# Kernel tuning notes

Hardware: AMD Instinct MI355X
Metric: run time of the kernel (lower is better)

## Reference

```python
import jax, jax.numpy as jnp
import numpy as np

N = 207      # nodes (hardcoded in source)
D = 128      # hid_dim
H = 8        # attention heads
C = D // H   # head dim
L = 4        # num_layers
B = 16       # batch
NO = 3       # number of orbits
SZ = 69      # orbit size
EPS = 1e-5
SLOPE = 0.2  # GATv2 leaky_relu negative slope


def _cat_matrix():
    # edge category for pair (i,j): off-diag -> pos_i*NO+pos_j, diag -> NO^2+pos_i
    pos = np.arange(N) // SZ
    c = pos[:, None] * NO + pos[None, :]
    np.fill_diagonal(c, NO * NO + pos)
    return c  # [N, N] int


def setup_inputs() -> dict:
    key = jax.random.key(0)
    ks = jax.random.split(key, 16)
    s = 0.05
    rn = lambda k, shape: jax.random.normal(k, shape, jnp.float32) * s
    return {
        "x": jax.random.normal(ks[0], (B, N, 6), jnp.float32),
        "cat": jnp.asarray(_cat_matrix(), jnp.int32),          # [N,N] edge categories
        "emb": rn(ks[1], (NO * NO + NO, D)),                   # edge embedding table
        "in1_W": rn(ks[2], (D, 6)), "in1_b": jnp.zeros((D,)),
        "ln1_g": jnp.ones((D,)), "ln1_b": jnp.zeros((D,)),
        "in2_W": rn(ks[3], (D, D)), "in2_b": jnp.zeros((D,)),
        "ln2_g": jnp.ones((D,)), "ln2_b": jnp.zeros((D,)),
        "Wl": rn(ks[4], (L, D, D)), "bl": jnp.zeros((L, D)),   # GATv2 lin_l (source)
        "Wr": rn(ks[5], (L, D, D)), "br": jnp.zeros((L, D)),   # GATv2 lin_r (target)
        "We": rn(ks[6], (L, D, D)),                            # GATv2 lin_edge (no bias)
        "att": rn(ks[7], (L, H, C)),                           # attention vector
        "cb": jnp.zeros((L, D)),                               # conv output bias
        "pW": rn(ks[8], (L, D, D)), "pb": jnp.zeros((L, D)),   # projection layers
        "lng": jnp.ones((L, D)), "lnb": jnp.zeros((L, D)),     # per-layer LayerNorm
        "oW": rn(ks[9], (2, D)), "ob": jnp.zeros((2,)),        # output layer
    }


def _ln(x, g, b):
    m = x.mean(-1, keepdims=True)
    v = ((x - m) ** 2).mean(-1, keepdims=True)
    return (x - m) * jax.lax.rsqrt(v + EPS) * g + b


def _fwd(cat, x, emb, in1_W, in1_b, ln1_g, ln1_b, in2_W, in2_b, ln2_g, ln2_b,
         Wl, bl, Wr, br, We, att, cb, pW, pb, lng, lnb, oW, ob):
    # input MLP: Linear -> LN -> ReLU -> Linear -> LN
    h = jax.nn.relu(_ln(x @ in1_W.T + in1_b, ln1_g, ln1_b))
    h = _ln(h @ in2_W.T + in2_b, ln2_g, ln2_b)                 # [B,N,D]
    e_all = emb[cat]                                           # [N,N,D] per-edge embedding
    for l in range(L):
        h_prev = h
        gs = (h @ Wl[l].T + bl[l]).reshape(B, N, H, C)         # source transform
        gd = (h @ Wr[l].T + br[l]).reshape(B, N, H, C)         # target transform
        ee = (e_all @ We[l].T).reshape(N, N, H, C)             # edge transform
        # per-edge GATv2 score: edge (i -> j), i source, j target
        z = jax.nn.leaky_relu(gs[:, :, None] + gd[:, None, :] + ee[None], SLOPE)  # [B,i,j,H,C]
        a = jnp.einsum('bijhc,hc->bijh', z, att[l])
        a = jax.nn.softmax(a, axis=1)                          # softmax over sources per target
        o = jnp.einsum('bijh,bihc->bjhc', a, gs).reshape(B, N, D) + cb[l]
        h = h_prev + jax.nn.relu(_ln(o @ pW[l].T + pb[l], lng[l], lnb[l]))
    return h @ oW.T + ob                                       # [B,N,2]


def reference(x, cat, emb, in1_W, in1_b, ln1_g, ln1_b, in2_W, in2_b, ln2_g, ln2_b,
              Wl, bl, Wr, br, We, att, cb, pW, pb, lng, lnb, oW, ob):
    return _fwd(cat, x, emb, in1_W, in1_b, ln1_g, ln1_b, in2_W, in2_b, ln2_g, ln2_b,
                Wl, bl, Wr, br, We, att, cb, pW, pb, lng, lnb, oW, ob)
```

## Files before the change

### kernel.cpp

```cpp
#include <hip/hip_runtime.h>
#include <hip/hip_bf16.h>

#define NN 207
#define DD 128
#define LL 4
#define BB 16
#define ROWS (BB*NN)
#define RB 8
#define LBLK (ROWS/RB)
#define EPSV 1e-5f
#define SLOPE 0.2f
#define GT4B (32*208*4)

#define BFBITS 0x3F803F80u

template<bool BF>
__device__ __forceinline__ float ldin(const void* p, int i) {
    if (BF) {
        unsigned short u = ((const unsigned short*)p)[i];
        return __uint_as_float(((unsigned)u) << 16);
    } else {
        return ((const float*)p)[i];
    }
}

template<bool BF>
__device__ __forceinline__ float4 ld4(const void* p, int q4) {
    if (BF) {
        uint2 u = ((const uint2*)p)[q4];
        float4 r;
        r.x = __uint_as_float(u.x << 16);
        r.y = __uint_as_float(u.x & 0xFFFF0000u);
        r.z = __uint_as_float(u.y << 16);
        r.w = __uint_as_float(u.y & 0xFFFF0000u);
        return r;
    } else {
        return ((const float4*)p)[q4];
    }
}

template<bool BF>
__device__ __forceinline__ void ldw32(const void* W, int base, float* w) {
    if (BF) {
        const uint4* p = (const uint4*)((const unsigned short*)W + base);
#pragma unroll
        for (int q = 0; q < 4; q++) {
            uint4 u = p[q];
            w[q*8+0] = __uint_as_float(u.x << 16);
            w[q*8+1] = __uint_as_float(u.x & 0xFFFF0000u);
            w[q*8+2] = __uint_as_float(u.y << 16);
            w[q*8+3] = __uint_as_float(u.y & 0xFFFF0000u);
            w[q*8+4] = __uint_as_float(u.z << 16);
            w[q*8+5] = __uint_as_float(u.z & 0xFFFF0000u);
            w[q*8+6] = __uint_as_float(u.w << 16);
            w[q*8+7] = __uint_as_float(u.w & 0xFFFF0000u);
        }
    } else {
        const float4* p = (const float4*)((const float*)W + base);
#pragma unroll
        for (int q = 0; q < 8; q++) {
            float4 u = p[q];
            w[q*4+0] = u.x; w[q*4+1] = u.y; w[q*4+2] = u.z; w[q*4+3] = u.w;
        }
    }
}

template<bool BF>
__device__ __forceinline__ float rowdot(const void* W, int rowbase, const float* sh) {
    float acc = 0.f;
    if (BF) {
        const uint4* p = (const uint4*)((const unsigned short*)W + rowbase);
#pragma unroll
        for (int q = 0; q < DD / 8; q++) {
            uint4 u = p[q];
            const float* s = sh + q * 8;
            acc += __uint_as_float(u.x << 16)        * s[0];
            acc += __uint_as_float(u.x & 0xFFFF0000u) * s[1];
            acc += __uint_as_float(u.y << 16)        * s[2];
            acc += __uint_as_float(u.y & 0xFFFF0000u) * s[3];
            acc += __uint_as_float(u.z << 16)        * s[4];
            acc += __uint_as_float(u.z & 0xFFFF0000u) * s[5];
            acc += __uint_as_float(u.w << 16)        * s[6];
            acc += __uint_as_float(u.w & 0xFFFF0000u) * s[7];
        }
    } else {
        const float4* p = (const float4*)((const float*)W + rowbase);
#pragma unroll
        for (int q = 0; q < DD / 4; q++) {
            float4 u = p[q];
            const float* s = sh + q * 4;
            acc += u.x * s[0]; acc += u.y * s[1]; acc += u.z * s[2]; acc += u.w * s[3];
        }
    }
    return acc;
}

template<bool BF>
__device__ void et_body(float* sh, const void* emb, const void* We, float* et) {
    int l = blockIdx.x / 12, c = blockIdx.x % 12, d = threadIdx.x;
    sh[d] = ldin<BF>(emb, c * DD + d);
    __syncthreads();
    et[(l * 12 + c) * DD + d] = rowdot<BF>(We, l * DD * DD + d * DD, sh);
}
__global__ void k_et(const unsigned* bits, const void* emb, const void* We, float* et) {
    __shared__ __align__(16) float smem[DD];
    if (bits[0] == BFBITS) et_body<true>(smem, emb, We, et);
    else                   et_body<false>(smem, emb, We, et);
}

#define LING_SMEM (RB*DD + RB*132 + 16 + RB*128)
template<bool BF>
__device__ void linG_body(float* smem, int hasPre, int epi, int hasNext,
                          const float* __restrict__ in,
                          const void* xin, const void* W1, const void* b1,
                          const void* g1, const void* bv1,
                          const void* W, int wOff,
                          const void* bias, const void* g, const void* bv, int dOff,
                          const void* Wl, const void* bl, const void* Wr, const void* br,
                          int nwOff, int nbOff,
                          float* __restrict__ h, float* __restrict__ gs,
                          float* __restrict__ gd, float* __restrict__ gs_t4,
                          const void* oW, const void* ob, void* out) {
    float* sh    = smem;
    float* so    = sh + RB * DD;
    float* stats = so + RB * 132;
    float* s_gs  = stats + 16;
    float* s_x   = s_gs;
    int r0 = blockIdx.x * RB;
    int t = threadIdx.x, d = t & 127, half = t >> 7;
    int rr2 = t >> 5, l32 = t & 31;

    if (hasPre) {
        if (t < RB * 6) s_x[t] = ldin<BF>(xin, r0 * 6 + t);
        __syncthreads();
        if (half == 0) {
            float w6[6];
#pragma unroll
            for (int k = 0; k < 6; k++) w6[k] = ldin<BF>(W1, d * 6 + k);
            float b0p = ldin<BF>(b1, d);
#pragma unroll
            for (int rr = 0; rr < RB; rr++) {
                float a = b0p;
#pragma unroll
                for (int k = 0; k < 6; k++) a += w6[k] * s_x[rr * 6 + k];
                so[rr * 132 + d] = a;
            }
        }
        __syncthreads();
        float s = 0.f, sq = 0.f;
#pragma unroll
        for (int k = 0; k < 4; k++) { float v = so[rr2 * 132 + l32 + 32 * k]; s += v; sq += v * v; }
        s += __shfl_xor(s, 1); s += __shfl_xor(s, 2); s += __shfl_xor(s, 4);
        s += __shfl_xor(s, 8); s += __shfl_xor(s, 16);
        sq += __shfl_xor(sq, 1); sq += __shfl_xor(sq, 2); sq += __shfl_xor(sq, 4);
        sq += __shfl_xor(sq, 8); sq += __shfl_xor(sq, 16);
        if (l32 == 0) {
            float mean = s * (1.f / DD);
            float var = sq * (1.f / DD) - mean * mean;
            stats[rr2 * 2] = mean; stats[rr2 * 2 + 1] = rsqrtf(var + EPSV);
        }
        __syncthreads();
        float gvp = ldin<BF>(g1, d), bbp = ldin<BF>(bv1, d);
#pragma unroll
        for (int rr = 0; rr < 4; rr++) {
            int row = half * 4 + rr;
            float v = (so[row * 132 + d] - stats[row * 2]) * stats[row * 2 + 1] * gvp + bbp;
            sh[row * DD + d] = fmaxf(v, 0.f);
        }
        __syncthreads();
    } else {
        ((float4*)sh)[t] = ((const float4*)(in + (size_t)r0 * DD))[t];
        __syncthreads();
    }

    float acc[4];
    float b0 = ldin<BF>(bias, dOff + d);
#pragma unroll
    for (int rr = 0; rr < 4; rr++) acc[rr] = b0;
#pragma unroll
    for (int c = 0; c < 4; c++) {
        float w[32];
        ldw32<BF>(W, wOff + d * DD + c * 32, w);
#pragma unroll
        for (int rr = 0; rr < 4; rr++) {
            const float* s = sh + (half * 4 + rr) * DD + c * 32;
            float a = acc[rr];
#pragma unroll
            for (int k = 0; k < 32; k++) a += s[k] * w[k];
            acc[rr] = a;
        }
    }
    __syncthreads();
#pragma unroll
    for (int rr = 0; rr < 4; rr++) so[(half * 4 + rr) * 132 + d] = acc[rr];
    __syncthreads();
    {
        float s = 0.f, sq = 0.f;
#pragma unroll
        for (int k = 0; k < 4; k++) { float v = so[rr2 * 132 + l32 + 32 * k]; s += v; sq += v * v; }
        s += __shfl_xor(s, 1); s += __shfl_xor(s, 2); s += __shfl_xor(s, 4);
        s += __shfl_xor(s, 8); s += __shfl_xor(s, 16);
        sq += __shfl_xor(sq, 1); sq += __shfl_xor(sq, 2); sq += __shfl_xor(sq, 4);
        sq += __shfl_xor(sq, 8); sq += __shfl_xor(sq, 16);
        if (l32 == 0) {
            float mean = s * (1.f / DD);
            float var = sq * (1.f / DD) - mean * mean;
            stats[rr2 * 2] = mean; stats[rr2 * 2 + 1] = rsqrtf(var + EPSV);
        }
    }
    __syncthreads();
    float gv = ldin<BF>(g, dOff + d), bb = ldin<BF>(bv, dOff + d);
#pragma unroll
    for (int rr = 0; rr < 4; rr++) {
        int row = half * 4 + rr;
        int rg = r0 + row;
        float v = (so[row * 132 + d] - stats[row * 2]) * stats[row * 2 + 1] * gv + bb;
        float hn;
        if (epi) hn = h[(size_t)rg * DD + d] + fmaxf(v, 0.f);
        else     hn = v;
        h[(size_t)rg * DD + d] = hn;
        sh[row * DD + d] = hn;
    }
    __syncthreads();
    if (!hasNext) {
        float s0 = 0.f, s1 = 0.f;
#pragma unroll
        for (int k = 0; k < 4; k++) {
            int dd = l32 + 32 * k;
            float hv = sh[rr2 * DD + dd];
            s0 += hv * ldin<BF>(oW, dd);
            s1 += hv * ldin<BF>(oW, DD + dd);
        }
        s0 += __shfl_xor(s0, 1); s0 += __shfl_xor(s0, 2); s0 += __shfl_xor(s0, 4);
        s0 += __shfl_xor(s0, 8); s0 += __shfl_xor(s0, 16);
        s1 += __shfl_xor(s1, 1); s1 += __shfl_xor(s1, 2); s1 += __shfl_xor(s1, 4);
        s1 += __shfl_xor(s1, 8); s1 += __shfl_xor(s1, 16);
        if (l32 == 0) {
            int rg = r0 + rr2;
            float v0 = s0 + ldin<BF>(ob, 0);
            float v1 = s1 + ldin<BF>(ob, 1);
            if (BF) {
                ((__hip_bfloat16*)out)[rg * 2 + 0] = __float2bfloat16(v0);
                ((__hip_bfloat16*)out)[rg * 2 + 1] = __float2bfloat16(v1);
            } else {
                ((float*)out)[rg * 2 + 0] = v0;
                ((float*)out)[rg * 2 + 1] = v1;
            }
        }
        return;
    }
    {
        const void* Wm = half ? Wr : Wl;
        const void* bm = half ? br : bl;
        float acc2[RB];
        float bn = ldin<BF>(bm, nbOff + d);
#pragma unroll
        for (int rr = 0; rr < RB; rr++) acc2[rr] = bn;
#pragma unroll
        for (int c = 0; c < 4; c++) {
            float w[32];
            ldw32<BF>(Wm, nwOff + d * DD + c * 32, w);
#pragma unroll
            for (int rr = 0; rr < RB; rr++) {
                const float* s = sh + rr * DD + c * 32;
                float a = acc2[rr];
#pragma unroll
                for (int k = 0; k < 32; k++) a += s[k] * w[k];
                acc2[rr] = a;
            }
        }
        if (half) {
#pragma unroll
            for (int rr = 0; rr < RB; rr++) gd[(size_t)(r0 + rr) * DD + d] = acc2[rr];
        } else {
#pragma unroll
            for (int rr = 0; rr < RB; rr++) {
                gs[(size_t)(r0 + rr) * DD + d] = acc2[rr];
                s_gs[rr * DD + d] = acc2[rr];
            }
        }
    }
    __syncthreads();
    {
        int d4 = t >> 3, iL = t & 7;
        int rg = r0 + iL;
        int bb2 = rg / NN, ii = rg - bb2 * NN;
        float4 v;
        v.x = s_gs[iL * DD + d4 * 4 + 0];
        v.y = s_gs[iL * DD + d4 * 4 + 1];
        v.z = s_gs[iL * DD + d4 * 4 + 2];
        v.w = s_gs[iL * DD + d4 * 4 + 3];
        ((float4*)(gs_t4 + (size_t)bb2 * GT4B))[d4 * 208 + ii] = v;
    }
}
__global__ void k_linG(const unsigned* bits, int hasPre, int epi, int hasNext,
                       const float* in,
                       const void* xin, const void* W1, const void* b1,
                       const void* g1, const void* bv1,
                       const void* W, int wOff,
                       const void* bias, const void* g, const void* bv, int dOff,
                       const void* Wl, const void* bl, const void* Wr, const void* br,
                       int nwOff, int nbOff,
                       float* h, float* gs, float* gd, float* gs_t4,
                       const void* oW, const void* ob, void* out) {
    __shared__ __align__(16) float smem[LING_SMEM];
    if (bits[0] == BFBITS)
        linG_body<true>(smem, hasPre, epi, hasNext, in, xin, W1, b1, g1, bv1,
                        W, wOff, bias, g, bv, dOff,
                        Wl, bl, Wr, br, nwOff, nbOff, h, gs, gd, gs_t4, oW, ob, out);
    else
        linG_body<false>(smem, hasPre, epi, hasNext, in, xin, W1, b1, g1, bv1,
                         W, wOff, bias, g, bv, dOff,
                         Wl, bl, Wr, br, nwOff, nbOff, h, gs, gd, gs_t4, oW, ob, out);
}

#define ATTN_SMEM (12*132 + 8*212 + 8 + 128 + 207)
template<bool BF>
__device__ void attn_body(float* smem, int l, const float* __restrict__ gs,
                          const float* __restrict__ gd, const float* __restrict__ et,
                          const float* __restrict__ gs_t4, const int* __restrict__ cat,
                          const void* att, const void* cb, float* __restrict__ o) {
    float* s_ge   = smem;
    float* s_pe   = s_ge + 12 * 132;
    float* s_inv  = s_pe + 8 * 212;
    float* s_part = s_inv + 8;
    int*   s_cat  = (int*)(s_part + 128);
    int p = blockIdx.x;
    int r = (p & 7) * (ROWS / 8) + (p >> 3);
    int t = threadIdx.x, d = t & 127, seg = t >> 7;
    int b = r / NN, j = r - b * NN;
    for (int idx = t; idx < NN; idx += 256) s_cat[idx] = cat[idx * NN + j];
    for (int idx = t; idx < 12 * DD; idx += 256) {
        int c = idx >> 7, k = idx & 127;
        s_ge[c * 132 + k] = et[l * 12 * DD + idx] + gd[(size_t)r * DD + k];
    }
    __syncthreads();
    const float* gsb = gs + (size_t)b * NN * DD;
    if (t < NN) {
        const float4* gt = ((const float4*)(gs_t4 + (size_t)b * GT4B)) + t;
        const float4* ge = (const float4*)(s_ge + s_cat[t] * 132);
        float acc[8];
#pragma unroll
        for (int hh = 0; hh < 8; hh++) acc[hh] = 0.f;
#pragma unroll
        for (int q = 0; q < 32; q++) {
            float4 g4 = gt[q * 208];
            float4 e4 = ge[q];
            float4 a4 = ld4<BF>(att, l * 32 + q);
            float z0 = g4.x + e4.x, z1 = g4.y + e4.y, z2 = g4.z + e4.z, z3 = g4.w + e4.w;
            z0 = fmaxf(z0, SLOPE * z0); z1 = fmaxf(z1, SLOPE * z1);
            z2 = fmaxf(z2, SLOPE * z2); z3 = fmaxf(z3, SLOPE * z3);
            acc[q >> 2] += a4.x * z0 + a4.y * z1 + a4.z * z2 + a4.w * z3;
        }
#pragma unroll
        for (int hh = 0; hh < 8; hh++) s_pe[hh * 212 + t] = acc[hh];
    }
    __syncthreads();
    if (t < 128) {
        int hh = t >> 4, l16 = t & 15;
        float vals[13]; float mx = -1e30f;
#pragma unroll
        for (int k = 0; k < 13; k++) {
            int i = l16 + 16 * k;
            vals[k] = (i < NN) ? s_pe[hh * 212 + i] : -1e30f;
            mx = fmaxf(mx, vals[k]);
        }
        mx = fmaxf(mx, __shfl_xor(mx, 1)); mx = fmaxf(mx, __shfl_xor(mx, 2));
        mx = fmaxf(mx, __shfl_xor(mx, 4)); mx = fmaxf(mx, __shfl_xor(mx, 8));
        float sum = 0.f;
#pragma unroll
        for (int k = 0; k < 13; k++) {
            int i = l16 + 16 * k;
            float e = (i < NN) ? __expf(vals[k] - mx) : 0.f;
            if (i < 208) s_pe[hh * 212 + i] = e;
            sum += e;
        }
        sum += __shfl_xor(sum, 1); sum += __shfl_xor(sum, 2);
        sum += __shfl_xor(sum, 4); sum += __shfl_xor(sum, 8);
        if (l16 == 0) s_inv[hh] = 1.f / sum;
    }
    __syncthreads();
    {
        int hh = d >> 4;
        const float* ep = s_pe + hh * 212;
        const float* gp = gsb + d;
        float a0 = 0.f, a1 = 0.f, a2 = 0.f, a3 = 0.f;
        int i = seg * 104;
        int iend = seg ? NN : 104;
        for (; i + 8 <= iend; i += 8) {
            float g0 = gp[(i+0)*DD], g1 = gp[(i+1)*DD], g2 = gp[(i+2)*DD], g3 = gp[(i+3)*DD];
            float g4 = gp[(i+4)*DD], g5 = gp[(i+5)*DD], g6 = gp[(i+6)*DD], g7 = gp[(i+7)*DD];
            a0 = fmaf(ep[i+0], g0, a0); a1 = fmaf(ep[i+1], g1, a1);
            a2 = fmaf(ep[i+2], g2, a2); a3 = fmaf(ep[i+3], g3, a3);
            a0 = fmaf(ep[i+4], g4, a0); a1 = fmaf(ep[i+5], g5, a1);
            a2 = fmaf(ep[i+6], g6, a2); a3 = fmaf(ep[i+7], g7, a3);
        }
        for (; i < iend; i++) a0 = fmaf(ep[i], gp[i * DD], a0);
        float part = a0 + a1 + a2 + a3;
        if (seg) s_part[d] = part;
        __syncthreads();
        if (!seg) o[(size_t)r * DD + d] = (part + s_part[d]) * s_inv[hh] + ldin<BF>(cb, l * DD + d);
    }
}
__global__ void __launch_bounds__(256, 4)
k_attn(const unsigned* bits, int l, const float* gs, const float* gd, const float* et,
       const float* gs_t4, const int* cat, const void* att, const void* cb,
       float* o) {
    __shared__ __align__(16) float smem[ATTN_SMEM];
    if (bits[0] == BFBITS) attn_body<true>(smem, l, gs, gd, et, gs_t4, cat, att, cb, o);
    else                   attn_body<false>(smem, l, gs, gd, et, gs_t4, cat, att, cb, o);
}

extern "C" void kernel_launch(void* const* d_in, const int* in_sizes, int n_in,
                              void* d_out, int out_size, void* d_ws, size_t ws_size,
                              hipStream_t stream) {
    const void* x     = d_in[0];
    const int*  cat   = (const int*)d_in[1];
    const void* emb   = d_in[2];
    const void* in1W  = d_in[3];
    const void* in1b  = d_in[4];
    const void* ln1g  = d_in[5];
    const void* ln1b  = d_in[6];
    const void* in2W  = d_in[7];
    const void* in2b  = d_in[8];
    const void* ln2g  = d_in[9];
    const void* ln2b  = d_in[10];
    const void* Wl    = d_in[11];
    const void* bl    = d_in[12];
    const void* Wr    = d_in[13];
    const void* br    = d_in[14];
    const void* We    = d_in[15];
    const void* att   = d_in[16];
    const void* cb    = d_in[17];
    const void* pW    = d_in[18];
    const void* pb    = d_in[19];
    const void* lng   = d_in[20];
    const void* lnb   = d_in[21];
    const void* oW    = d_in[22];
    const void* ob    = d_in[23];

    const unsigned* bits = (const unsigned*)ln1g;

    float* ws  = (float*)d_ws;
    float* h     = ws + 16;
    float* gs    = h    + ROWS * DD;
    float* gd    = gs   + ROWS * DD;
    float* o     = gd   + ROWS * DD;
    float* et    = o    + ROWS * DD;
    float* gs_t4 = et   + LL * 12 * DD;

    k_et<<<LL * 12, DD, 0, stream>>>(bits, emb, We, et);
    k_linG<<<LBLK, 256, 0, stream>>>(bits, 1, 0, 1, (const float*)nullptr,
                                     x, in1W, in1b, ln1g, ln1b,
                                     in2W, 0, in2b, ln2g, ln2b, 0,
                                     Wl, bl, Wr, br, 0, 0,
                                     h, gs, gd, gs_t4, oW, ob, d_out);
    for (int l = 0; l < LL; l++) {
        k_attn<<<ROWS, 256, 0, stream>>>(bits, l, gs, gd, et, gs_t4, cat, att, cb, o);
        k_linG<<<LBLK, 256, 0, stream>>>(bits, 0, 1, (l < LL - 1) ? 1 : 0, o,
                                         x, in1W, in1b, ln1g, ln1b,
                                         pW, l * DD * DD, pb, lng, lnb, l * DD,
                                         Wl, bl, Wr, br, (l + 1) * DD * DD, (l + 1) * DD,
                                         h, gs, gd, gs_t4, oW, ob, d_out);
    }
}
```

Measured before the change: 334.7 us.

## Pre-transpose linear weights to fp32 k-major layout for coalesced loads

Adds a prologue kernel that transposes the in2, projection, lin_l and lin_r weights into a float workspace laid out [k][d]. The linG matmuls then read one weight per k that is coalesced across threads, with activations read as float4 from shared memory. Previously each thread loaded its own 128-wide weight row, so accesses were strided across the wavefront. This costs one extra launch and extra workspace memory per call, and in the bf16 case it doubles the bytes read per weight.

```diff
diff --git a/kernel.cpp b/kernel.cpp
--- a/kernel.cpp
+++ b/kernel.cpp
@@ -11,6 +11,7 @@
 #define EPSV 1e-5f
 #define SLOPE 0.2f
 #define GT4B (32*208*4)
+#define WTM  16384
 
 #define BFBITS 0x3F803F80u
 
@@ -40,32 +41,6 @@
 }
 
 template<bool BF>
-__device__ __forceinline__ void ldw32(const void* W, int base, float* w) {
-    if (BF) {
-        const uint4* p = (const uint4*)((const unsigned short*)W + base);
-#pragma unroll
-        for (int q = 0; q < 4; q++) {
-            uint4 u = p[q];
-            w[q*8+0] = __uint_as_float(u.x << 16);
-            w[q*8+1] = __uint_as_float(u.x & 0xFFFF0000u);
-            w[q*8+2] = __uint_as_float(u.y << 16);
-            w[q*8+3] = __uint_as_float(u.y & 0xFFFF0000u);
-            w[q*8+4] = __uint_as_float(u.z << 16);
-            w[q*8+5] = __uint_as_float(u.z & 0xFFFF0000u);
-            w[q*8+6] = __uint_as_float(u.w << 16);
-            w[q*8+7] = __uint_as_float(u.w & 0xFFFF0000u);
-        }
-    } else {
-        const float4* p = (const float4*)((const float*)W + base);
-#pragma unroll
-        for (int q = 0; q < 8; q++) {
-            float4 u = p[q];
-            w[q*4+0] = u.x; w[q*4+1] = u.y; w[q*4+2] = u.z; w[q*4+3] = u.w;
-        }
-    }
-}
-
-template<bool BF>
 __device__ __forceinline__ float rowdot(const void* W, int rowbase, const float* sh) {
     float acc = 0.f;
     if (BF) {
@@ -96,6 +71,23 @@
 }
 
 template<bool BF>
+__device__ void wt_body(const void* in2W, const void* pW, const void* Wl, const void* Wr,
+                        float* wt) {
+    int m = blockIdx.x >> 7, k = blockIdx.x & 127, d = threadIdx.x;
+    const void* src; int off;
+    if (m == 0)      { src = in2W; off = 0; }
+    else if (m <= 4) { src = pW;  off = (m - 1) * WTM; }
+    else if (m <= 8) { src = Wl;  off = (m - 5) * WTM; }
+    else             { src = Wr;  off = (m - 9) * WTM; }
+    wt[m * WTM + k * DD + d] = ldin<BF>(src, off + d * DD + k);
+}
+__global__ void k_wt(const unsigned* bits, const void* in2W, const void* pW,
+                     const void* Wl, const void* Wr, float* wt) {
+    if (bits[0] == BFBITS) wt_body<true>(in2W, pW, Wl, Wr, wt);
+    else                   wt_body<false>(in2W, pW, Wl, Wr, wt);
+}
+
+template<bool BF>
 __device__ void et_body(float* sh, const void* emb, const void* We, float* et) {
     int l = blockIdx.x / 12, c = blockIdx.x % 12, d = threadIdx.x;
     sh[d] = ldin<BF>(emb, c * DD + d);
@@ -114,10 +106,9 @@
                           const float* __restrict__ in,
                           const void* xin, const void* W1, const void* b1,
                           const void* g1, const void* bv1,
-                          const void* W, int wOff,
+                          const float* __restrict__ wt, int mA,
                           const void* bias, const void* g, const void* bv, int dOff,
-                          const void* Wl, const void* bl, const void* Wr, const void* br,
-                          int nwOff, int nbOff,
+                          int mL, int mR, const void* bl, const void* br, int nbOff,
                           float* __restrict__ h, float* __restrict__ gs,
                           float* __restrict__ gd, float* __restrict__ gs_t4,
                           const void* oW, const void* ob, void* out) {
@@ -173,21 +164,26 @@
         __syncthreads();
     }
 
+    const float* WT = wt + mA * WTM;
     float acc[4];
     float b0 = ldin<BF>(bias, dOff + d);
 #pragma unroll
     for (int rr = 0; rr < 4; rr++) acc[rr] = b0;
-#pragma unroll
-    for (int c = 0; c < 4; c++) {
-        float w[32];
-        ldw32<BF>(W, wOff + d * DD + c * 32, w);
-#pragma unroll
-        for (int rr = 0; rr < 4; rr++) {
-            const float* s = sh + (half * 4 + rr) * DD + c * 32;
-            float a = acc[rr];
-#pragma unroll
-            for (int k = 0; k < 32; k++) a += s[k] * w[k];
-            acc[rr] = a;
+    {
+        const float* xr = sh + half * 4 * DD;
+        for (int k4 = 0; k4 < 32; k4++) {
+            float4 xa = *(const float4*)(xr + 0 * DD + k4 * 4);
+            float4 xb = *(const float4*)(xr + 1 * DD + k4 * 4);
+            float4 xc = *(const float4*)(xr + 2 * DD + k4 * 4);
+            float4 xd = *(const float4*)(xr + 3 * DD + k4 * 4);
+            float w0 = WT[(k4 * 4 + 0) * DD + d];
+            float w1 = WT[(k4 * 4 + 1) * DD + d];
+            float w2 = WT[(k4 * 4 + 2) * DD + d];
+            float w3 = WT[(k4 * 4 + 3) * DD + d];
+            acc[0] += w0 * xa.x + w1 * xa.y + w2 * xa.z + w3 * xa.w;
+            acc[1] += w0 * xb.x + w1 * xb.y + w2 * xb.z + w3 * xb.w;
+            acc[2] += w0 * xc.x + w1 * xc.y + w2 * xc.z + w3 * xc.w;
+            acc[3] += w0 * xd.x + w1 * xd.y + w2 * xd.z + w3 * xd.w;
         }
     }
     __syncthreads();
@@ -250,24 +246,33 @@
         return;
     }
     {
-        const void* Wm = half ? Wr : Wl;
+        const float* WTm = wt + (half ? mR : mL) * WTM;
         const void* bm = half ? br : bl;
         float acc2[RB];
         float bn = ldin<BF>(bm, nbOff + d);
 #pragma unroll
         for (int rr = 0; rr < RB; rr++) acc2[rr] = bn;
-#pragma unroll
-        for (int c = 0; c < 4; c++) {
-            float w[32];
-            ldw32<BF>(Wm, nwOff + d * DD + c * 32, w);
-#pragma unroll
-            for (int rr = 0; rr < RB; rr++) {
-                const float* s = sh + rr * DD + c * 32;
-                float a = acc2[rr];
-#pragma unroll
-                for (int k = 0; k < 32; k++) a += s[k] * w[k];
-                acc2[rr] = a;
-            }
+        for (int k4 = 0; k4 < 32; k4++) {
+            float4 x0 = *(const float4*)(sh + 0 * DD + k4 * 4);
+            float4 x1 = *(const float4*)(sh + 1 * DD + k4 * 4);
+            float4 x2 = *(const float4*)(sh + 2 * DD + k4 * 4);
+            float4 x3 = *(const float4*)(sh + 3 * DD + k4 * 4);
+            float4 x4 = *(const float4*)(sh + 4 * DD + k4 * 4);
+            float4 x5 = *(const float4*)(sh + 5 * DD + k4 * 4);
+            float4 x6 = *(const float4*)(sh + 6 * DD + k4 * 4);
+            float4 x7 = *(const float4*)(sh + 7 * DD + k4 * 4);
+            float w0 = WTm[(k4 * 4 + 0) * DD + d];
+            float w1 = WTm[(k4 * 4 + 1) * DD + d];
+            float w2 = WTm[(k4 * 4 + 2) * DD + d];
+            float w3 = WTm[(k4 * 4 + 3) * DD + d];
+            acc2[0] += w0 * x0.x + w1 * x0.y + w2 * x0.z + w3 * x0.w;
+            acc2[1] += w0 * x1.x + w1 * x1.y + w2 * x1.z + w3 * x1.w;
+            acc2[2] += w0 * x2.x + w1 * x2.y + w2 * x2.z + w3 * x2.w;
+            acc2[3] += w0 * x3.x + w1 * x3.y + w2 * x3.z + w3 * x3.w;
+            acc2[4] += w0 * x4.x + w1 * x4.y + w2 * x4.z + w3 * x4.w;
+            acc2[5] += w0 * x5.x + w1 * x5.y + w2 * x5.z + w3 * x5.w;
+            acc2[6] += w0 * x6.x + w1 * x6.y + w2 * x6.z + w3 * x6.w;
+            acc2[7] += w0 * x7.x + w1 * x7.y + w2 * x7.z + w3 * x7.w;
         }
         if (half) {
 #pragma unroll
@@ -297,21 +302,20 @@
                        const float* in,
                        const void* xin, const void* W1, const void* b1,
                        const void* g1, const void* bv1,
-                       const void* W, int wOff,
+                       const float* wt, int mA,
                        const void* bias, const void* g, const void* bv, int dOff,
-                       const void* Wl, const void* bl, const void* Wr, const void* br,
-                       int nwOff, int nbOff,
+                       int mL, int mR, const void* bl, const void* br, int nbOff,
                        float* h, float* gs, float* gd, float* gs_t4,
                        const void* oW, const void* ob, void* out) {
     __shared__ __align__(16) float smem[LING_SMEM];
     if (bits[0] == BFBITS)
         linG_body<true>(smem, hasPre, epi, hasNext, in, xin, W1, b1, g1, bv1,
-                        W, wOff, bias, g, bv, dOff,
-                        Wl, bl, Wr, br, nwOff, nbOff, h, gs, gd, gs_t4, oW, ob, out);
+                        wt, mA, bias, g, bv, dOff, mL, mR, bl, br, nbOff,
+                        h, gs, gd, gs_t4, oW, ob, out);
     else
         linG_body<false>(smem, hasPre, epi, hasNext, in, xin, W1, b1, g1, bv1,
-                         W, wOff, bias, g, bv, dOff,
-                         Wl, bl, Wr, br, nwOff, nbOff, h, gs, gd, gs_t4, oW, ob, out);
+                         wt, mA, bias, g, bv, dOff, mL, mR, bl, br, nbOff,
+                         h, gs, gd, gs_t4, oW, ob, out);
 }
 
 #define ATTN_SMEM (12*132 + 8*212 + 8 + 128 + 207)
@@ -448,19 +452,21 @@
     float* o     = gd   + ROWS * DD;
     float* et    = o    + ROWS * DD;
     float* gs_t4 = et   + LL * 12 * DD;
-
+    float* wt    = gs_t4 + (size_t)BB * GT4B;
+
+    k_wt<<<13 * 128, 128, 0, stream>>>(bits, in2W, pW, Wl, Wr, wt);
     k_et<<<LL * 12, DD, 0, stream>>>(bits, emb, We, et);
     k_linG<<<LBLK, 256, 0, stream>>>(bits, 1, 0, 1, (const float*)nullptr,
                                      x, in1W, in1b, ln1g, ln1b,
-                                     in2W, 0, in2b, ln2g, ln2b, 0,
-                                     Wl, bl, Wr, br, 0, 0,
+                                     wt, 0, in2b, ln2g, ln2b, 0,
+                                     5, 9, bl, br, 0,
                                      h, gs, gd, gs_t4, oW, ob, d_out);
     for (int l = 0; l < LL; l++) {
         k_attn<<<ROWS, 256, 0, stream>>>(bits, l, gs, gd, et, gs_t4, cat, att, cb, o);
         k_linG<<<LBLK, 256, 0, stream>>>(bits, 0, 1, (l < LL - 1) ? 1 : 0, o,
                                          x, in1W, in1b, ln1g, ln1b,
-                                         pW, l * DD * DD, pb, lng, lnb, l * DD,
-                                         Wl, bl, Wr, br, (l + 1) * DD * DD, (l + 1) * DD,
+                                         wt, 1 + l, pb, lng, lnb, l * DD,
+                                         5 + (l + 1), 9 + (l + 1), bl, br, (l + 1) * DD,
                                          h, gs, gd, gs_t4, oW, ob, d_out);
     }
 }
```

Measured after the change: 323.3 us. 1.04x faster.
